# Optimization experiments

Measured on AMD Instinct MI355X. Metric: run time of the kernel, lower is better.

The kernel has to match this reference:

```python
import jax, jax.numpy as jnp
import numpy as np

B, N, D, H, L = 512, 50000, 64, 600, 200
ALPHA = 1.0
EPS_NORM = 1e-12


def _l2n(x):
    # matches tf.linalg.l2_normalize / keras.backend.l2_normalize (axis=-1)
    return x * jax.lax.rsqrt(jnp.maximum(jnp.sum(x * x, axis=-1, keepdims=True), EPS_NORM))


def setup_inputs() -> dict:
    key = jax.random.key(0)
    ks = jax.random.split(key, 8)
    inputs = jax.random.randint(ks[0], (B, N), 0, 2).astype(jnp.float32)
    item_emb = jax.random.normal(ks[1], (N, D), jnp.float32) * 0.1
    W1 = jax.random.normal(ks[2], (N + D, H), jnp.float32) * 0.01
    Wm = jax.random.normal(ks[3], (H, L), jnp.float32) * 0.05
    Wv = jax.random.normal(ks[4], (H, L), jnp.float32) * 0.05
    Wd1 = jax.random.normal(ks[5], (L, H), jnp.float32) * 0.05
    Wd2 = jax.random.normal(ks[6], (H, N), jnp.float32) * 0.01
    eps = jax.random.normal(ks[7], (B, L), jnp.float32)
    return {
        "inputs": inputs, "item_emb": item_emb,
        "W1": W1, "b1": jnp.zeros((H,), jnp.float32),
        "Wm": Wm, "bm": jnp.zeros((L,), jnp.float32),
        "Wv": Wv, "bv": jnp.zeros((L,), jnp.float32),
        "Wd1": Wd1, "bd1": jnp.zeros((H,), jnp.float32),
        "Wd2": Wd2, "bd2": jnp.zeros((N,), jnp.float32),
        "eps": eps,
    }


def reference(inputs, item_emb, W1, b1, Wm, bm, Wv, bv, Wd1, bd1, Wd2, bd2, eps):
    # --- vectorized replacement of tf.map_fn row-wise masked gather + mean pool ---
    mask = (inputs > 0).astype(inputs.dtype)            # [B, N]
    cnt = jnp.maximum(jnp.sum(mask, axis=-1, keepdims=True), 1.0)
    pooled = (mask @ item_emb) / cnt                    # [B, D] mean of selected item embeddings
    x = jnp.concatenate([inputs, ALPHA * _l2n(pooled)], axis=-1)  # [B, N+D]
    # --- encoder ---
    xn = _l2n(x)                                        # l2 normalize over axis=1
    h = jnp.tanh(xn @ W1 + b1)                          # [B, H]
    z_mean = h @ Wm + bm                                # [B, L]
    z_log_var = h @ Wv + bv                             # [B, L]
    z = z_mean + jnp.exp(0.5 * z_log_var) * eps         # reparameterization
    # --- decoder ---
    reconstructed = jnp.tanh(z @ Wd1 + bd1) @ Wd2 + bd2  # [B, N]
    kl_loss = -0.5 * jnp.mean(z_log_var - jnp.square(z_mean) - jnp.exp(z_log_var) + 1.0)
    return reconstructed, kl_loss
```

## Files before the change

### kernel.cpp

```cpp
#include <hip/hip_runtime.h>

#define BB 512
#define NN 50000
#define DD 64
#define HH 600
#define LL 200

#define K1 50176
#define S1 1568
#define N1P 704
#define KCH 49

#define K2 608
#define N2P 50048

typedef __attribute__((ext_vector_type(8))) short bf16x8;
typedef __attribute__((ext_vector_type(4))) float f32x4;

__device__ __forceinline__ unsigned short f2bf(float f) {
  union { float f; unsigned u; } v; v.f = f;
  unsigned r = v.u + 0x7fffu + ((v.u >> 16) & 1u);
  return (unsigned short)(r >> 16);
}

__global__ __launch_bounds__(256) void k_prep(const float* __restrict__ inp,
                                              unsigned* __restrict__ mask,
                                              float* __restrict__ cnt,
                                              float* __restrict__ P,
                                              float* __restrict__ outkl) {
  int b = blockIdx.x, tid = threadIdx.x;
  const float4* row4 = (const float4*)(inp + (size_t)b * NN);
  unsigned* mrow = mask + (size_t)b * S1;
  int c = 0;
  for (int w = tid; w < S1; w += 256) {
    unsigned m = 0;
    int kb = w * 32;
    if (kb + 32 <= NN) {
#pragma unroll
      for (int q = 0; q < 8; ++q) {
        float4 f = row4[w * 8 + q];
        m |= (f.x > 0.5f ? 1u : 0u) << (4 * q);
        m |= (f.y > 0.5f ? 1u : 0u) << (4 * q + 1);
        m |= (f.z > 0.5f ? 1u : 0u) << (4 * q + 2);
        m |= (f.w > 0.5f ? 1u : 0u) << (4 * q + 3);
      }
    } else {
      for (int k = kb; k < NN && k < kb + 32; ++k)
        m |= (inp[(size_t)b * NN + k] > 0.5f ? 1u : 0u) << (k - kb);
    }
    mrow[w] = m;
    c += __popc(m);
  }
  __shared__ int sred[256];
  sred[tid] = c; __syncthreads();
  for (int s = 128; s > 0; s >>= 1) { if (tid < s) sred[tid] += sred[tid + s]; __syncthreads(); }
  if (tid == 0) cnt[b] = (float)sred[0];
  for (int j = tid; j < N1P; j += 256) P[(size_t)b * N1P + j] = 0.f;
  if (b == 0 && tid == 0) *outkl = 0.f;
}

__global__ __launch_bounds__(256) void k_convB1(const float* __restrict__ W1,
                                                const float* __restrict__ item_emb,
                                                unsigned short* __restrict__ BT) {
  __shared__ unsigned short lds[64][65];
  int k0 = blockIdx.x * 64, j0 = blockIdx.y * 64;
  int tx = threadIdx.x & 63, ty = threadIdx.x >> 6;
  int j = j0 + tx;
#pragma unroll
  for (int r = 0; r < 16; ++r) {
    int k = k0 + ty + 4 * r;
    float v = 0.f;
    if (k < NN) {
      if (j < HH) v = W1[(size_t)k * HH + j];
      else if (j < HH + DD) v = item_emb[(size_t)k * DD + (j - HH)];
    }
    lds[tx][ty + 4 * r] = f2bf(v);
  }
  __syncthreads();
#pragma unroll
  for (int r = 0; r < 16; ++r) {
    int jj = j0 + ty + 4 * r;
    int kk = k0 + tx;
    BT[(size_t)jj * K1 + kk] = lds[ty + 4 * r][tx];
  }
}

__global__ __launch_bounds__(256) void k_convB2(const float* __restrict__ Wd2,
                                                unsigned short* __restrict__ WT) {
  __shared__ unsigned short lds[64][65];
  int n0 = blockIdx.x * 64, k0 = blockIdx.y * 64;
  int tx = threadIdx.x & 63, ty = threadIdx.x >> 6;
  int n = n0 + tx;
#pragma unroll
  for (int r = 0; r < 16; ++r) {
    int k = k0 + ty + 4 * r;
    float v = 0.f;
    if (k < HH && n < NN) v = Wd2[(size_t)k * NN + n];
    lds[tx][ty + 4 * r] = f2bf(v);
  }
  __syncthreads();
#pragma unroll
  for (int r = 0; r < 16; ++r) {
    int nn = n0 + ty + 4 * r;
    int kk = k0 + tx;
    if (kk < K2) WT[(size_t)nn * K2 + kk] = lds[ty + 4 * r][tx];
  }
}

__global__ __launch_bounds__(512) void k_gemm1(const unsigned* __restrict__ mask,
                                               const unsigned short* __restrict__ BT,
                                               float* __restrict__ P) {
  int wave = threadIdx.x >> 6, lane = threadIdx.x & 63;
  int n0 = blockIdx.x * 64;
  int m0 = wave * 64;
  int lr = lane & 15, kg = lane >> 4;

  const unsigned short* bp = BT + (size_t)(n0 + lr) * K1 + kg * 8;

  f32x4 acc[4][4] = {};
  int s0 = blockIdx.y * KCH, s1 = s0 + KCH;

  union AU { unsigned u[4]; bf16x8 v; };

  for (int s = s0; s < s1; ++s) {
    int kb = s * 32;
    bf16x8 b[4];
#pragma unroll
    for (int j = 0; j < 4; ++j)
      b[j] = *(const bf16x8*)(bp + (size_t)j * 16 * K1 + kb);

    bf16x8 a[4];
#pragma unroll
    for (int i = 0; i < 4; ++i) {
      unsigned mw = mask[(size_t)(m0 + i * 16 + lr) * S1 + s];
      unsigned byte = (mw >> (kg * 8)) & 0xFFu;
      AU au;
#pragma unroll
      for (int p = 0; p < 4; ++p) {
        unsigned t = (byte >> (2 * p)) & 3u;
        t = (t | (t << 15)) & 0x10001u;
        au.u[p] = t * 0x3F80u;
      }
      a[i] = au.v;
    }

#pragma unroll
    for (int i = 0; i < 4; ++i)
#pragma unroll
      for (int j = 0; j < 4; ++j)
        acc[i][j] = __builtin_amdgcn_mfma_f32_16x16x32_bf16(a[i], b[j], acc[i][j], 0, 0, 0);
  }

  int row0 = (lane >> 4) * 4, col = lane & 15;
#pragma unroll
  for (int i = 0; i < 4; ++i)
#pragma unroll
    for (int j = 0; j < 4; ++j)
#pragma unroll
      for (int r = 0; r < 4; ++r)
        atomicAdd(&P[(size_t)(m0 + i * 16 + row0 + r) * N1P + (n0 + j * 16 + col)], acc[i][j][r]);
}

__global__ __launch_bounds__(256) void k_mid(const float* __restrict__ P,
                                             const float* __restrict__ cntb,
                                             const float* __restrict__ W1,
                                             const float* __restrict__ b1,
                                             const float* __restrict__ Wm,
                                             const float* __restrict__ bm,
                                             const float* __restrict__ Wv,
                                             const float* __restrict__ bv,
                                             const float* __restrict__ Wd1,
                                             const float* __restrict__ bd1,
                                             const float* __restrict__ eps,
                                             unsigned short* __restrict__ TB,
                                             float* __restrict__ outkl) {
  int b = blockIdx.x, tid = threadIdx.x;
  __shared__ float pn[DD];
  __shared__ float h[HH];
  __shared__ float z[LL];
  __shared__ float red[1];
  __shared__ float sred[256];

  float cnt = cntb[b];
  if (tid < 64) {
    float pooled = P[(size_t)b * N1P + HH + tid] / fmaxf(cnt, 1.f);
    float s2 = pooled * pooled;
    for (int o = 32; o > 0; o >>= 1) s2 += __shfl_xor(s2, o);
    float pnv = pooled * rsqrtf(fmaxf(s2, 1e-12f));
    pn[tid] = pnv;
    float p2 = pnv * pnv;
    for (int o = 32; o > 0; o >>= 1) p2 += __shfl_xor(p2, o);
    if (tid == 0) red[0] = rsqrtf(fmaxf(cnt + p2, 1e-12f));
  }
  __syncthreads();
  float inv = red[0];

  for (int j = tid; j < HH; j += 256) {
    float corr = 0.f;
#pragma unroll 8
    for (int d = 0; d < DD; ++d) corr += pn[d] * W1[(size_t)(NN + d) * HH + j];
    h[j] = tanhf((P[(size_t)b * N1P + j] + corr) * inv + b1[j]);
  }
  __syncthreads();

  float klp = 0.f;
  for (int l = tid; l < LL; l += 256) {
    float zm = bm[l], zv = bv[l];
    for (int j = 0; j < HH; ++j) {
      float hv = h[j];
      zm += hv * Wm[(size_t)j * LL + l];
      zv += hv * Wv[(size_t)j * LL + l];
    }
    z[l] = zm + expf(0.5f * zv) * eps[(size_t)b * LL + l];
    klp += zv - zm * zm - expf(zv) + 1.f;
  }
  sred[tid] = klp; __syncthreads();
  for (int s = 128; s > 0; s >>= 1) { if (tid < s) sred[tid] += sred[tid + s]; __syncthreads(); }
  if (tid == 0) atomicAdd(outkl, sred[0] * (-0.5f / (float)(BB * LL)));

  for (int j = tid; j < K2; j += 256) {
    unsigned short o = 0;
    if (j < HH) {
      float acc = bd1[j];
      for (int l = 0; l < LL; ++l) acc += z[l] * Wd1[(size_t)l * HH + j];
      o = f2bf(tanhf(acc));
    }
    TB[(size_t)b * K2 + j] = o;
  }
}

__global__ __launch_bounds__(512) void k_gemm2(const unsigned short* __restrict__ T,
                                               const unsigned short* __restrict__ WT,
                                               const float* __restrict__ bd2,
                                               float* __restrict__ out) {
  int wave = threadIdx.x >> 6, lane = threadIdx.x & 63;
  int n0 = blockIdx.x * 64;
  int m0 = wave * 64;
  int lr = lane & 15, lk = (lane >> 4) * 8;

  const unsigned short* ap = T + (size_t)(m0 + lr) * K2 + lk;
  const unsigned short* bp = WT + (size_t)(n0 + lr) * K2 + lk;

  f32x4 acc[4][4] = {};
#pragma unroll
  for (int ks = 0; ks < K2 / 32; ++ks) {
    int kb = ks * 32;
    bf16x8 a[4], b[4];
#pragma unroll
    for (int i = 0; i < 4; ++i) a[i] = *(const bf16x8*)(ap + (size_t)i * 16 * K2 + kb);
#pragma unroll
    for (int i = 0; i < 4; ++i) b[i] = *(const bf16x8*)(bp + (size_t)i * 16 * K2 + kb);
#pragma unroll
    for (int i = 0; i < 4; ++i)
#pragma unroll
      for (int j = 0; j < 4; ++j)
        acc[i][j] = __builtin_amdgcn_mfma_f32_16x16x32_bf16(a[i], b[j], acc[i][j], 0, 0, 0);
  }

  int row0 = (lane >> 4) * 4, col = lane & 15;
#pragma unroll
  for (int i = 0; i < 4; ++i)
#pragma unroll
    for (int j = 0; j < 4; ++j) {
      int n = n0 + j * 16 + col;
      if (n < NN) {
        float bias = bd2[n];
#pragma unroll
        for (int r = 0; r < 4; ++r) {
          int m = m0 + i * 16 + row0 + r;
          out[(size_t)m * NN + n] = acc[i][j][r] + bias;
        }
      }
    }
}

extern "C" void kernel_launch(void* const* d_in, const int* in_sizes, int n_in,
                              void* d_out, int out_size, void* d_ws, size_t ws_size,
                              hipStream_t stream) {
  (void)in_sizes; (void)n_in; (void)out_size; (void)ws_size;
  const float* inputs   = (const float*)d_in[0];
  const float* item_emb = (const float*)d_in[1];
  const float* W1  = (const float*)d_in[2];
  const float* b1  = (const float*)d_in[3];
  const float* Wm  = (const float*)d_in[4];
  const float* bm  = (const float*)d_in[5];
  const float* Wv  = (const float*)d_in[6];
  const float* bv  = (const float*)d_in[7];
  const float* Wd1 = (const float*)d_in[8];
  const float* bd1 = (const float*)d_in[9];
  const float* Wd2 = (const float*)d_in[10];
  const float* bd2 = (const float*)d_in[11];
  const float* eps = (const float*)d_in[12];
  float* out = (float*)d_out;

  char* ws = (char*)d_ws;
  unsigned* mask      = (unsigned*)(ws + 0ull);
  unsigned short* BT1 = (unsigned short*)(ws + 3211264ull);
  unsigned short* W2T = (unsigned short*)(ws + 73859072ull);
  float* P            = (float*)(ws + 134717440ull);
  unsigned short* TB  = (unsigned short*)(ws + 136159232ull);
  float* cnt          = (float*)(ws + 136781824ull);

  float* outkl = out + (size_t)BB * NN;

  k_prep  <<<dim3(BB),       dim3(256), 0, stream>>>(inputs, mask, cnt, P, outkl);
  k_convB1<<<dim3(784, 11),  dim3(256), 0, stream>>>(W1, item_emb, BT1);
  k_convB2<<<dim3(782, 10),  dim3(256), 0, stream>>>(Wd2, W2T);
  k_gemm1 <<<dim3(11, 32),   dim3(512), 0, stream>>>(mask, BT1, P);
  k_mid   <<<dim3(BB),       dim3(256), 0, stream>>>(P, cnt, W1, b1, Wm, bm, Wv, bv, Wd1, bd1, eps, TB, outkl);
  k_gemm2 <<<dim3(782),      dim3(512), 0, stream>>>(TB, W2T, bd2, out);
}
```

Baseline: 799.3 us.

## Stage GEMM operands through swizzled LDS with double-buffered async global-to-LDS loads

Both GEMMs now copy B tiles into LDS with global_load_lds, using an XOR swizzle and double buffering so the next K-stage loads while MFMAs run on the current one. The mask is stored transposed (word-major over batch) so gemm1 can stage it into LDS in one contiguous load, and the K-split changes from 32 to 28 chunks. gemm2's K is padded to 640 so it splits into 128-wide stages. The cost is extra LDS use, barriers and hand-written vmcnt waits, and k_prep now does strided mask writes.

```diff
diff --git a/kernel.cpp b/kernel.cpp
--- a/kernel.cpp
+++ b/kernel.cpp
@@ -9,9 +9,12 @@
 #define K1 50176
 #define S1 1568
 #define N1P 704
-#define KCH 49
-
-#define K2 608
+#define NCH 28
+#define CKE 1792
+#define CW 56
+#define NST 14
+
+#define K2P 640
 #define N2P 50048
 
 typedef __attribute__((ext_vector_type(8))) short bf16x8;
@@ -23,14 +26,18 @@
   return (unsigned short)(r >> 16);
 }
 
+__device__ __forceinline__ void g2l16(const void* g, void* l) {
+  __builtin_amdgcn_global_load_lds((const __attribute__((address_space(1))) unsigned int*)g,
+                                   (__attribute__((address_space(3))) unsigned int*)l, 16, 0, 0);
+}
+
 __global__ __launch_bounds__(256) void k_prep(const float* __restrict__ inp,
-                                              unsigned* __restrict__ mask,
+                                              unsigned* __restrict__ maskT,
                                               float* __restrict__ cnt,
                                               float* __restrict__ P,
                                               float* __restrict__ outkl) {
   int b = blockIdx.x, tid = threadIdx.x;
   const float4* row4 = (const float4*)(inp + (size_t)b * NN);
-  unsigned* mrow = mask + (size_t)b * S1;
   int c = 0;
   for (int w = tid; w < S1; w += 256) {
     unsigned m = 0;
@@ -48,7 +55,7 @@
       for (int k = kb; k < NN && k < kb + 32; ++k)
         m |= (inp[(size_t)b * NN + k] > 0.5f ? 1u : 0u) << (k - kb);
     }
-    mrow[w] = m;
+    maskT[(size_t)w * BB + b] = m;
     c += __popc(m);
   }
   __shared__ int sred[256];
@@ -103,52 +110,80 @@
   for (int r = 0; r < 16; ++r) {
     int nn = n0 + ty + 4 * r;
     int kk = k0 + tx;
-    if (kk < K2) WT[(size_t)nn * K2 + kk] = lds[ty + 4 * r][tx];
-  }
-}
-
-__global__ __launch_bounds__(512) void k_gemm1(const unsigned* __restrict__ mask,
+    WT[(size_t)nn * K2P + kk] = lds[ty + 4 * r][tx];
+  }
+}
+
+__global__ __launch_bounds__(512) void k_gemm1(const unsigned* __restrict__ maskT,
                                                const unsigned short* __restrict__ BT,
                                                float* __restrict__ P) {
-  int wave = threadIdx.x >> 6, lane = threadIdx.x & 63;
+  __shared__ unsigned short sB[2 * 8192];
+  __shared__ unsigned sM[2 * 2048];
+  int tid = threadIdx.x;
+  int wave = tid >> 6, lane = tid & 63;
+  int lr = lane & 15, kg = lane >> 4;
   int n0 = blockIdx.x * 64;
   int m0 = wave * 64;
-  int lr = lane & 15, kg = lane >> 4;
-
-  const unsigned short* bp = BT + (size_t)(n0 + lr) * K1 + kg * 8;
-
+  int cK = blockIdx.y * CKE;
+  int cWo = blockIdx.y * CW;
+
+  auto stage = [&](int p, int st) {
+    int kb = cK + st * 128;
+#pragma unroll
+    for (int i = 0; i < 2; ++i) {
+      int row = wave * 8 + i * 4 + kg;
+      int cbs = (lr * 16) ^ ((row & 7) << 4);
+      const unsigned short* src = BT + (size_t)(n0 + row) * K1 + kb + (cbs >> 1);
+      unsigned short* dst = sB + p * 8192 + wave * 1024 + i * 512;
+      g2l16(src, dst);
+    }
+    int w0 = cWo + st * 4;
+    const unsigned* msrc = maskT + (size_t)w0 * BB + wave * 256 + lane * 4;
+    unsigned* mdst = sM + p * 2048 + wave * 256;
+    g2l16(msrc, mdst);
+  };
+
+  stage(0, 0);
   f32x4 acc[4][4] = {};
-  int s0 = blockIdx.y * KCH, s1 = s0 + KCH;
-
-  union AU { unsigned u[4]; bf16x8 v; };
-
-  for (int s = s0; s < s1; ++s) {
-    int kb = s * 32;
-    bf16x8 b[4];
-#pragma unroll
-    for (int j = 0; j < 4; ++j)
-      b[j] = *(const bf16x8*)(bp + (size_t)j * 16 * K1 + kb);
-
-    bf16x8 a[4];
-#pragma unroll
-    for (int i = 0; i < 4; ++i) {
-      unsigned mw = mask[(size_t)(m0 + i * 16 + lr) * S1 + s];
-      unsigned byte = (mw >> (kg * 8)) & 0xFFu;
-      AU au;
-#pragma unroll
-      for (int p = 0; p < 4; ++p) {
-        unsigned t = (byte >> (2 * p)) & 3u;
-        t = (t | (t << 15)) & 0x10001u;
-        au.u[p] = t * 0x3F80u;
-      }
-      a[i] = au.v;
-    }
-
-#pragma unroll
-    for (int i = 0; i < 4; ++i)
-#pragma unroll
-      for (int j = 0; j < 4; ++j)
-        acc[i][j] = __builtin_amdgcn_mfma_f32_16x16x32_bf16(a[i], b[j], acc[i][j], 0, 0, 0);
+
+  for (int st = 0; st < NST; ++st) {
+    int cur = st & 1;
+    if (st + 1 < NST) {
+      stage(cur ^ 1, st + 1);
+      asm volatile("s_waitcnt vmcnt(3)" ::: "memory");
+    } else {
+      asm volatile("s_waitcnt vmcnt(0)" ::: "memory");
+    }
+    __builtin_amdgcn_s_barrier();
+
+    const unsigned short* Bb = sB + cur * 8192;
+    const unsigned* Mb = sM + cur * 2048;
+#pragma unroll
+    for (int ks = 0; ks < 4; ++ks) {
+      bf16x8 b[4];
+#pragma unroll
+      for (int j = 0; j < 4; ++j) {
+        int row = j * 16 + lr;
+        int cb = (ks * 64 + kg * 16) ^ ((row & 7) << 4);
+        b[j] = *(const bf16x8*)(Bb + row * 128 + (cb >> 1));
+      }
+#pragma unroll
+      for (int i = 0; i < 4; ++i) {
+        unsigned mw = Mb[ks * 512 + m0 + i * 16 + lr];
+        unsigned byt = (mw >> (kg * 8)) & 0xFFu;
+        union { unsigned u[4]; bf16x8 v; } au;
+#pragma unroll
+        for (int p2 = 0; p2 < 4; ++p2) {
+          unsigned t = (byt >> (2 * p2)) & 3u;
+          t = (t | (t << 15)) & 0x10001u;
+          au.u[p2] = t * 0x3F80u;
+        }
+#pragma unroll
+        for (int j = 0; j < 4; ++j)
+          acc[i][j] = __builtin_amdgcn_mfma_f32_16x16x32_bf16(au.v, b[j], acc[i][j], 0, 0, 0);
+      }
+    }
+    __builtin_amdgcn_s_barrier();
   }
 
   int row0 = (lane >> 4) * 4, col = lane & 15;
@@ -218,14 +253,14 @@
   for (int s = 128; s > 0; s >>= 1) { if (tid < s) sred[tid] += sred[tid + s]; __syncthreads(); }
   if (tid == 0) atomicAdd(outkl, sred[0] * (-0.5f / (float)(BB * LL)));
 
-  for (int j = tid; j < K2; j += 256) {
+  for (int j = tid; j < K2P; j += 256) {
     unsigned short o = 0;
     if (j < HH) {
       float acc = bd1[j];
       for (int l = 0; l < LL; ++l) acc += z[l] * Wd1[(size_t)l * HH + j];
       o = f2bf(tanhf(acc));
     }
-    TB[(size_t)b * K2 + j] = o;
+    TB[(size_t)b * K2P + j] = o;
   }
 }
 
@@ -233,28 +268,58 @@
                                                const unsigned short* __restrict__ WT,
                                                const float* __restrict__ bd2,
                                                float* __restrict__ out) {
-  int wave = threadIdx.x >> 6, lane = threadIdx.x & 63;
+  __shared__ unsigned short sB[2 * 8192];
+  int tid = threadIdx.x;
+  int wave = tid >> 6, lane = tid & 63;
+  int lr = lane & 15, kg = lane >> 4;
   int n0 = blockIdx.x * 64;
   int m0 = wave * 64;
-  int lr = lane & 15, lk = (lane >> 4) * 8;
-
-  const unsigned short* ap = T + (size_t)(m0 + lr) * K2 + lk;
-  const unsigned short* bp = WT + (size_t)(n0 + lr) * K2 + lk;
-
+
+  auto stage = [&](int p, int st) {
+    int kb = st * 128;
+#pragma unroll
+    for (int i = 0; i < 2; ++i) {
+      int row = wave * 8 + i * 4 + kg;
+      int cbs = (lr * 16) ^ ((row & 7) << 4);
+      const unsigned short* src = WT + (size_t)(n0 + row) * K2P + kb + (cbs >> 1);
+      unsigned short* dst = sB + p * 8192 + wave * 1024 + i * 512;
+      g2l16(src, dst);
+    }
+  };
+
+  stage(0, 0);
   f32x4 acc[4][4] = {};
-#pragma unroll
-  for (int ks = 0; ks < K2 / 32; ++ks) {
-    int kb = ks * 32;
-    bf16x8 a[4], b[4];
-#pragma unroll
-    for (int i = 0; i < 4; ++i) a[i] = *(const bf16x8*)(ap + (size_t)i * 16 * K2 + kb);
-#pragma unroll
-    for (int i = 0; i < 4; ++i) b[i] = *(const bf16x8*)(bp + (size_t)i * 16 * K2 + kb);
-#pragma unroll
-    for (int i = 0; i < 4; ++i)
-#pragma unroll
-      for (int j = 0; j < 4; ++j)
-        acc[i][j] = __builtin_amdgcn_mfma_f32_16x16x32_bf16(a[i], b[j], acc[i][j], 0, 0, 0);
+
+  for (int st = 0; st < 5; ++st) {
+    int cur = st & 1;
+    if (st + 1 < 5) {
+      stage(cur ^ 1, st + 1);
+      asm volatile("s_waitcnt vmcnt(2)" ::: "memory");
+    } else {
+      asm volatile("s_waitcnt vmcnt(0)" ::: "memory");
+    }
+    __builtin_amdgcn_s_barrier();
+
+    const unsigned short* Bb = sB + cur * 8192;
+#pragma unroll
+    for (int ks = 0; ks < 4; ++ks) {
+      bf16x8 a[4], b[4];
+#pragma unroll
+      for (int i = 0; i < 4; ++i)
+        a[i] = *(const bf16x8*)(T + (size_t)(m0 + i * 16 + lr) * K2P + st * 128 + ks * 32 + kg * 8);
+#pragma unroll
+      for (int j = 0; j < 4; ++j) {
+        int row = j * 16 + lr;
+        int cb = (ks * 64 + kg * 16) ^ ((row & 7) << 4);
+        b[j] = *(const bf16x8*)(Bb + row * 128 + (cb >> 1));
+      }
+#pragma unroll
+      for (int i = 0; i < 4; ++i)
+#pragma unroll
+        for (int j = 0; j < 4; ++j)
+          acc[i][j] = __builtin_amdgcn_mfma_f32_16x16x32_bf16(a[i], b[j], acc[i][j], 0, 0, 0);
+    }
+    __builtin_amdgcn_s_barrier();
   }
 
   int row0 = (lane >> 4) * 4, col = lane & 15;
@@ -294,19 +359,19 @@
   float* out = (float*)d_out;
 
   char* ws = (char*)d_ws;
-  unsigned* mask      = (unsigned*)(ws + 0ull);
+  unsigned* maskT     = (unsigned*)(ws + 0ull);
   unsigned short* BT1 = (unsigned short*)(ws + 3211264ull);
   unsigned short* W2T = (unsigned short*)(ws + 73859072ull);
-  float* P            = (float*)(ws + 134717440ull);
-  unsigned short* TB  = (unsigned short*)(ws + 136159232ull);
-  float* cnt          = (float*)(ws + 136781824ull);
+  float* P            = (float*)(ws + 137920512ull);
+  unsigned short* TB  = (unsigned short*)(ws + 139362304ull);
+  float* cnt          = (float*)(ws + 140017664ull);
 
   float* outkl = out + (size_t)BB * NN;
 
-  k_prep  <<<dim3(BB),       dim3(256), 0, stream>>>(inputs, mask, cnt, P, outkl);
+  k_prep  <<<dim3(BB),       dim3(256), 0, stream>>>(inputs, maskT, cnt, P, outkl);
   k_convB1<<<dim3(784, 11),  dim3(256), 0, stream>>>(W1, item_emb, BT1);
   k_convB2<<<dim3(782, 10),  dim3(256), 0, stream>>>(Wd2, W2T);
-  k_gemm1 <<<dim3(11, 32),   dim3(512), 0, stream>>>(mask, BT1, P);
+  k_gemm1 <<<dim3(11, NCH),  dim3(512), 0, stream>>>(maskT, BT1, P);
   k_mid   <<<dim3(BB),       dim3(256), 0, stream>>>(P, cnt, W1, b1, Wm, bm, Wv, bv, Wd1, bd1, eps, TB, outkl);
   k_gemm2 <<<dim3(782),      dim3(512), 0, stream>>>(TB, W2T, bd2, out);
 }
```

Result: faster. 704.4 us (-11.9%).
